# Performance work log

Hardware: AMD Instinct MI355X
Metric: run time of the kernel (lower is better)

Reference implementation:

```python
import jax, jax.numpy as jnp
import numpy as np

NEG = -1e30  # log-space 'zero' (avoid actual -inf for stable grads)
BLANK = 1


def _ctc_single(logp, target, il, tl):
    # logp: [T, V] log-probabilities; target: [S] int; il, tl: scalar lengths
    T, V = logp.shape
    S = target.shape[0]
    L = 2 * S + 1
    # extended label sequence: blank, t0, blank, t1, ..., blank
    ext = jnp.full((L,), BLANK, dtype=target.dtype).at[1::2].set(target)
    prev2 = jnp.concatenate([jnp.full((2,), -1, dtype=ext.dtype), ext[:-2]])
    can_skip = (ext != BLANK) & (ext != prev2)  # allowed s-2 transition
    valid = jnp.arange(L) < (2 * tl + 1)  # mask lattice positions beyond target length
    lp_ext = logp[:, ext]  # [T, L] gather of emission log-probs along the lattice

    alpha0 = jnp.full((L,), NEG, dtype=logp.dtype)
    alpha0 = alpha0.at[0].set(lp_ext[0, 0]).at[1].set(lp_ext[0, 1])
    alpha0 = jnp.where(valid, alpha0, NEG)

    def step(alpha, inp):
        t, lp = inp  # lp: [L]
        a1 = jnp.concatenate([jnp.full((1,), NEG, alpha.dtype), alpha[:-1]])
        a2 = jnp.concatenate([jnp.full((2,), NEG, alpha.dtype), alpha[:-2]])
        a2 = jnp.where(can_skip, a2, NEG)
        new = jnp.logaddexp(jnp.logaddexp(alpha, a1), a2) + lp
        new = jnp.where(valid, new, NEG)
        new = jnp.where(t < il, new, alpha)  # freeze alpha past input length
        return new, None

    alpha, _ = jax.lax.scan(step, alpha0, (jnp.arange(1, T), lp_ext[1:]))
    end = 2 * tl
    ll = jnp.logaddexp(alpha[end], alpha[end - 1])
    loss = -ll
    # zero_infinity=True: clamp non-finite / degenerate losses to 0
    loss = jnp.where(loss < 1e29, loss, 0.0)
    return loss


def setup_inputs() -> dict:
    key = jax.random.key(0)
    k1, k2, k3, k4 = jax.random.split(key, 4)
    B, T, V, S = 64, 2000, 256, 400
    # module expects log-probabilities over phonemes
    log_probs = jax.nn.log_softmax(
        jax.random.normal(k1, (B, T, V), dtype=jnp.float32), axis=-1)
    # targets avoid blank_id=1 (labels in [2, V))
    targets = jax.random.randint(k2, (B, S), 2, V, dtype=jnp.int32)
    input_lengths = jax.random.randint(k3, (B,), T // 2, T + 1, dtype=jnp.int32)
    target_lengths = jax.random.randint(k4, (B,), S // 2, S + 1, dtype=jnp.int32)
    return {"log_probs": log_probs, "targets": targets,
            "input_lengths": input_lengths, "target_lengths": target_lengths}


def reference(log_probs, targets, input_lengths, target_lengths):
    losses = jax.vmap(_ctc_single)(log_probs, targets, input_lengths, target_lengths)
    # nn.CTCLoss reduction='mean': per-sample loss divided by target length, then batch mean
    return jnp.mean(losses / target_lengths.astype(losses.dtype))
```

## Files before the change

kernel.cpp:

```cpp
#include <hip/hip_runtime.h>

#define LOG2E 1.4426950408889634f
#define LN2   0.6931471805599453f

namespace {
constexpr int B    = 64;
constexpr int T    = 2000;
constexpr int V    = 256;
constexpr int S    = 400;
constexpr int CHK  = 8;
constexpr int NCTP = 250;
constexpr int KP   = 408;
constexpr size_t GELEM  = (size_t)B * NCTP * KP * 8;
constexpr size_t GBYTES = GELEM * 2;
constexpr size_t LAOFF  = GBYTES / 4;
constexpr size_t LGOFF  = LAOFF + 64 * 1024;
constexpr size_t REQBYTES = GBYTES + 2 * 64 * 1024 * 4;
constexpr int LSTR = 260;
constexpr int NW7  = 7;
constexpr int NCT7 = 250;
constexpr int BST7 = 12;
}

using h8 = __attribute__((ext_vector_type(8))) _Float16;

__device__ __forceinline__ float fexp2(float x){ return __builtin_amdgcn_exp2f(x); }
__device__ __forceinline__ float flog2(float x){ return __builtin_amdgcn_logf(x); }

__device__ __forceinline__ float wave_shr1(float x) {
  int v = __builtin_amdgcn_update_dpp(0, __builtin_bit_cast(int, x),
                                      0x138, 0xf, 0xf, true);
  return __builtin_bit_cast(float, v);
}
__device__ __forceinline__ int wave_shr1_i(int x) {
  return __builtin_amdgcn_update_dpp(0, x, 0x138, 0xf, 0xf, true);
}
__device__ __forceinline__ float wave_shl1(float x) {
  int v = __builtin_amdgcn_update_dpp(0, __builtin_bit_cast(int, x),
                                      0x130, 0xf, 0xf, true);
  return __builtin_bit_cast(float, v);
}
__device__ __forceinline__ int wave_shl1_i(int x) {
  return __builtin_amdgcn_update_dpp(0, x, 0x130, 0xf, 0xf, true);
}

__global__ __launch_bounds__(512)
void ctc_gather_kernel(const float* __restrict__ logp,
                       const int* __restrict__ targets,
                       _Float16* __restrict__ G)
{
  const int tile = blockIdx.x;
  const int b    = blockIdx.y;
  const int tid  = threadIdx.x;
  const int i0   = tile * 64;
  const float* lp = logp + (size_t)b * T * V;
  const int*   tg = targets + (size_t)b * S;

  __shared__ float ls[64 * LSTR];
  __shared__ int   tgs[S];

  for (int f = tid; f < 64 * 64; f += 512) {
    const int row = f >> 6, c4 = f & 63;
    int t = i0 + 1 + row; if (t > T - 1) t = T - 1;
    float4 v = ((const float4*)(lp + (size_t)t * V))[c4];
    *(float4*)&ls[row * LSTR + c4 * 4] = v;
  }
  for (int k = tid; k < S; k += 512) tgs[k] = tg[k];
  __syncthreads();

  const int w    = tid >> 6;
  const int lane = tid & 63;
  _Float16* gb = G + (size_t)b * NCTP * KP * 8;

  for (int it = w; it < 64; it += 8) {
    const int cc = it >> 3;
    const int j  = it & 7;
    const int c  = tile * 8 + cc;
    if (c >= NCTP) continue;
    if (lane > 50) continue;
    const int k = 8 * lane + j;
    const int e = (k < S) ? tgs[k] : 1;
    h8 hv;
    #pragma unroll
    for (int jj = 0; jj < 8; ++jj)
      hv[jj] = (_Float16)fexp2(ls[(cc * 8 + jj) * LSTR + e] * LOG2E);
    *(h8*)(gb + ((size_t)c * KP + j * 51 + lane) * 8) = hv;
  }
}

__global__ __launch_bounds__(64)
void ctc_fb_kernel(const float* __restrict__ logp,
                   const int* __restrict__ targets,
                   const int* __restrict__ input_len,
                   const int* __restrict__ target_len,
                   const _Float16* __restrict__ G,
                   float* __restrict__ la,
                   float* __restrict__ lg)
{
  const int b    = blockIdx.x;
  const int dir  = blockIdx.y;
  const int lane = threadIdx.x & 63;
  const float* __restrict__ lp = logp + (size_t)b * T * V;
  const int il = input_len[b];
  const int tl = target_len[b];
  const int m  = il >> 1;
  const int* tg = targets + (size_t)b * S;

  const _Float16* Gb = G + (size_t)b * NCTP * KP * 8;
  const int lclamp = (lane < 50) ? lane : 50;

  float skF[8], skB[8];
  #pragma unroll
  for (int j = 0; j < 8; ++j) {
    const int k   = 8 * lane + j;
    const int kc  = k < S ? k : S - 1;
    const int km  = (k - 1) < 0 ? 0 : ((k - 1) < S ? (k - 1) : S - 1);
    skF[j] = (k > 0 && tg[kc] != tg[km]) ? 1.0f : 0.0f;
    const int k2  = k + 1;
    const int k2c = k2 < S ? k2 : S - 1;
    const int k2m = (k2 - 1) < S ? (k2 - 1) : S - 1;
    skB[j] = (tg[k2c] != tg[k2m]) ? 1.0f : 0.0f;
  }

  h8 bufA[9], bufB[9];

  auto loadch = [&](h8 (&buf)[9], int c2) {
    if (c2 < 0) c2 = 0;
    if (c2 > NCTP - 1) c2 = NCTP - 1;
    const _Float16* src = Gb + (size_t)c2 * (KP * 8);
    #pragma unroll
    for (int j = 0; j < 8; ++j)
      buf[j] = *(const h8*)(src + (size_t)(j * 51 + lclamp) * 8);
    buf[8] = *(const h8*)(src + (size_t)50 * 8);
  };

  if (dir == 0) {
    float a[16];
    #pragma unroll
    for (int i = 0; i < 16; ++i) a[i] = 0.0f;
    int  E = 0;
    bool alive = (lane == 0);
    if (lane == 0) {
      a[0] = fexp2(lp[1] * LOG2E);
      a[1] = fexp2(lp[tg[0]] * LOG2E);
    }

    auto fwd_sub = [&](h8 (&buf)[9], const int c_) {
      h8 cur[9];
      #pragma unroll
      for (int r = 0; r < 9; ++r) cur[r] = buf[r];
      loadch(buf, c_ + 2);

      const int E1 = wave_shr1_i(E);
      if (!alive) E = E1;
      int d = E1 - E; d = d > 126 ? 126 : (d < -126 ? -126 : d);
      const float f = ldexpf(1.0f, d);

      #pragma unroll
      for (int i = 0; i < 8; ++i) {
        const int t = 1 + c_ * CHK + i;
        if (t <= m) {
          const float pbi = (float)cur[8][i];
          const float h = wave_shr1(a[15]) * f;
          #pragma unroll
          for (int j = 7; j >= 0; --j) {
            const float psj = (float)cur[j][i];
            const float lo = j ? a[2 * j - 1] : h;
            a[2 * j + 1] = __builtin_fmaf(lo, skF[j],
                                          a[2 * j + 1] + a[2 * j]) * psj;
            a[2 * j]     = (a[2 * j] + lo) * pbi;
          }
        }
      }
      {
        float mx[8];
        #pragma unroll
        for (int q = 0; q < 8; ++q) mx[q] = fmaxf(a[2 * q], a[2 * q + 1]);
        #pragma unroll
        for (int q = 0; q < 4; ++q) mx[q] = fmaxf(mx[q], mx[q + 4]);
        const float m2 = fmaxf(fmaxf(mx[0], mx[1]), fmaxf(mx[2], mx[3]));
        int k = 0; (void)frexpf(m2, &k);
        #pragma unroll
        for (int i = 0; i < 16; ++i) a[i] = ldexpf(a[i], -k);
        E += k;
        alive = (m2 != 0.0f);
      }
    };

    loadch(bufA, 0); loadch(bufB, 1);
    const int NCH = (m + 7) >> 3;
    for (int c = 0; c < NCH; c += 2) {
      fwd_sub(bufA, c);
      fwd_sub(bufB, c + 1);
    }

    float* dst = la + (size_t)b * 1024 + 16 * lane;
    #pragma unroll
    for (int i = 0; i < 16; ++i) dst[i] = flog2(a[i]) + (float)E;
  } else {
    float g[16];
    const int s0 = 16 * lane;
    bool alive = false;
    #pragma unroll
    for (int i = 0; i < 16; ++i) {
      const int s = s0 + i;
      g[i] = (s == 2 * tl || s == 2 * tl - 1) ? 1.0f : 0.0f;
      alive = alive || (g[i] != 0.0f);
    }
    int E = 0;

    const int c_hi = (il - 2) >> 3;
    const int c_lo = m >> 3;

    auto bwd_sub = [&](h8 (&buf)[9], const int c_) {
      h8 cur[9];
      #pragma unroll
      for (int r = 0; r < 9; ++r) cur[r] = buf[r];
      loadch(buf, c_ - 2);

      const int E1 = wave_shl1_i(E);
      if (!alive) E = E1;
      int d = E1 - E; d = d > 126 ? 126 : (d < -126 ? -126 : d);
      const float f = ldexpf(1.0f, d);

      #pragma unroll
      for (int ii = 0; ii < 8; ++ii) {
        const int i = 7 - ii;
        const int row = 1 + c_ * CHK + i;
        if (row > m && row < il) {
          const float pbi = (float)cur[8][i];
          float pg[16];
          #pragma unroll
          for (int q = 0; q < 8; ++q) {
            pg[2 * q]     = g[2 * q]     * pbi;
            pg[2 * q + 1] = g[2 * q + 1] * (float)cur[q][i];
          }
          const float h0 = wave_shl1(pg[0]) * f;
          const float h1 = wave_shl1(pg[1]) * f;
          #pragma unroll
          for (int q = 0; q < 8; ++q) {
            const float u1 = (q < 7) ? pg[2 * q + 2] : h0;
            const float u2 = (q < 7) ? pg[2 * q + 3] : h1;
            g[2 * q + 1] = __builtin_fmaf(u2, skB[q], pg[2 * q + 1] + u1);
            g[2 * q]     = pg[2 * q] + pg[2 * q + 1];
          }
        }
      }
      {
        float mx[8];
        #pragma unroll
        for (int q = 0; q < 8; ++q) mx[q] = fmaxf(g[2 * q], g[2 * q + 1]);
        #pragma unroll
        for (int q = 0; q < 4; ++q) mx[q] = fmaxf(mx[q], mx[q + 4]);
        const float m2 = fmaxf(fmaxf(mx[0], mx[1]), fmaxf(mx[2], mx[3]));
        int k = 0; (void)frexpf(m2, &k);
        #pragma unroll
        for (int i = 0; i < 16; ++i) g[i] = ldexpf(g[i], -k);
        E += k;
        alive = (m2 != 0.0f);
      }
    };

    loadch(bufA, c_hi); loadch(bufB, c_hi - 1);
    for (int c = c_hi; c >= c_lo; c -= 2) {
      bwd_sub(bufA, c);
      bwd_sub(bufB, c - 1);
    }

    float* dst = lg + (size_t)b * 1024 + 16 * lane;
    #pragma unroll
    for (int i = 0; i < 16; ++i) dst[i] = flog2(g[i]) + (float)E;
  }
}

__global__ __launch_bounds__(64)
void ctc_merge_kernel(const float* __restrict__ la,
                      const float* __restrict__ lg,
                      const int* __restrict__ target_len,
                      float* __restrict__ out)
{
  const int b    = blockIdx.x;
  const int lane = threadIdx.x;
  const int tl = target_len[b];
  const int Lb = 2 * tl + 1;
  const float* A  = la + (size_t)b * 1024;
  const float* Gm = lg + (size_t)b * 1024;

  float vs[16];
  float vmax = -1e30f;
  #pragma unroll
  for (int r = 0; r < 16; ++r) {
    const int s = lane + 64 * r;
    float x = A[s] + Gm[s];
    x = (s < Lb) ? x : -1e30f;
    vs[r] = x;
    vmax = fmaxf(vmax, x);
  }
  #pragma unroll
  for (int o = 32; o > 0; o >>= 1) vmax = fmaxf(vmax, __shfl_xor(vmax, o, 64));
  float sum = 0.0f;
  #pragma unroll
  for (int r = 0; r < 16; ++r) sum += fexp2(vs[r] - vmax);
  #pragma unroll
  for (int o = 32; o > 0; o >>= 1) sum += __shfl_xor(sum, o, 64);
  if (lane == 0) {
    const float ll = (vmax + flog2(sum)) * LN2;
    float loss = -ll;
    if (!(loss < 1e29f)) loss = 0.0f;
    atomicAdd(out, loss / ((float)tl * (float)B));
  }
}

__global__ __launch_bounds__(NW7 * 64)
void ctc_alpha7_kernel(const float* __restrict__ logp,
                       const int* __restrict__ targets,
                       const int* __restrict__ input_len,
                       const int* __restrict__ target_len,
                       float* __restrict__ out)
{
  const int b    = blockIdx.x;
  const int tid  = threadIdx.x;
  const int w    = tid >> 6;
  const int lane = tid & 63;
  const bool lane0 = (lane == 0);
  const float* __restrict__ lp = logp + (size_t)b * T * V;
  const int il = input_len[b];
  const int tl = target_len[b];
  const int Lb = 2 * tl + 1;

  __shared__ float bnd[NW7 - 1][NCT7 * BST7];
  __shared__ int   cnt[NW7 - 1];
  __shared__ float pblk[T];
  __shared__ float afin[NW7 * 64 * 2];

  if (tid < NW7 - 1) cnt[tid] = 0;

  const int* tg = targets + (size_t)b * S;
  const int k1 = (tid < S) ? tid : (S - 1);
  const int e1 = tg[k1];
  const float sk1 = (k1 == 0 || e1 != tg[k1 - 1]) ? 1.0f : 0.0f;

  for (int i = tid; i < T; i += NW7 * 64) {
    int t = (i + 1 < T) ? (i + 1) : (T - 1);
    pblk[i] = fexp2(lp[(size_t)t * V + 1] * LOG2E);
  }
  __syncthreads();

  const bool active = (w * 128) < Lb;
  if (active) {
    float a0 = 0.0f, a1 = 0.0f;
    int   E  = 0;
    if (tid == 0) { a0 = fexp2(lp[1] * LOG2E); a1 = fexp2(lp[e1] * LOG2E); }

    float tokL[CHK];
    #pragma unroll
    for (int i = 0; i < CHK; ++i) tokL[i] = lp[(size_t)(1 + i) * V + e1];

    const int NCH = (il - 1 + CHK - 1) / CHK;
    for (int c = 0; c < NCH; ++c) {
      const int t0 = 1 + c * CHK;
      float tokP[CHK];
      #pragma unroll
      for (int i = 0; i < CHK; ++i) tokP[i] = fexp2(tokL[i] * LOG2E);
      float nl[CHK];
      if (c + 1 < NCT7) {
        #pragma unroll
        for (int i = 0; i < CHK; ++i) {
          int tt = t0 + CHK + i; if (tt > T - 1) tt = T - 1;
          nl[i] = lp[(size_t)tt * V + e1];
        }
      }
      float pbk[CHK];
      {
        float4 q0 = *(const float4*)&pblk[c * CHK];
        float4 q1 = *(const float4*)&pblk[c * CHK + 4];
        pbk[0]=q0.x; pbk[1]=q0.y; pbk[2]=q0.z; pbk[3]=q0.w;
        pbk[4]=q1.x; pbk[5]=q1.y; pbk[6]=q1.z; pbk[7]=q1.w;
      }
      float bq[CHK];
      int Ep = 0;
      if (w > 0) {
        while (__hip_atomic_load(&cnt[w - 1], __ATOMIC_ACQUIRE,
                                 __HIP_MEMORY_SCOPE_WORKGROUP) < c + 1)
          __builtin_amdgcn_s_sleep(1);
        const float* src = &bnd[w - 1][c * BST7];
        float4 q0 = *(const float4*)(src);
        float4 q1 = *(const float4*)(src + 4);
        bq[0]=q0.x; bq[1]=q0.y; bq[2]=q0.z; bq[3]=q0.w;
        bq[4]=q1.x; bq[5]=q1.y; bq[6]=q1.z; bq[7]=q1.w;
        Ep = __float_as_int(src[8]);
      } else {
        #pragma unroll
        for (int i = 0; i < CHK; ++i) bq[i] = 0.0f;
      }
      const float mz  = fmaxf(a0, a1);
      const int   E1o = __shfl_up(E, 1);
      const int   E8  = __shfl_up(E, 8);
      const int   E9  = __shfl_up(E, 9);
      const float mz1 = __shfl_up(mz, 1);
      if (mz == 0.0f) E = (lane < 8) ? Ep : E8;
      int E1 = (mz1 == 0.0f) ? ((lane <= 8) ? Ep : E9) : E1o;
      if (lane0) E1 = (w == 0) ? E : Ep;
      int d = E1 - E; d = d > 126 ? 126 : (d < -126 ? -126 : d);
      const float f = ldexpf(1.0f, d);
      const float a1s = a1;
      float pub[CHK];
      #pragma unroll
      for (int i = 0; i < CHK; ++i) {
        const int t = t0 + i;
        if (t < il) {
          float hl = wave_shr1(a1);
          hl = lane0 ? bq[i] : hl;
          hl *= f;
          float s01 = a1 + a0;
          a1 = __builtin_fmaf(hl, sk1, s01) * tokP[i];
          a0 = (a0 + hl) * pbk[i];
        }
        pub[i] = a1;
      }
      if (w < NW7 - 1 && lane == 63) {
        float* dst = &bnd[w][c * BST7];
        dst[0] = a1s;
        #pragma unroll
        for (int i = 0; i < CHK - 1; ++i) dst[1 + i] = pub[i];
        dst[8] = __int_as_float(E);
        __hip_atomic_store(&cnt[w], c + 1, __ATOMIC_RELEASE,
                           __HIP_MEMORY_SCOPE_WORKGROUP);
      }
      {
        float m2 = fmaxf(a0, a1);
        int k = 0;
        (void)frexpf(m2, &k);
        a0 = ldexpf(a0, -k);
        a1 = ldexpf(a1, -k);
        E += k;
      }
      #pragma unroll
      for (int i = 0; i < CHK; ++i) tokL[i] = nl[i];
    }
    afin[2 * tid]     = flog2(a0) + (float)E;
    afin[2 * tid + 1] = flog2(a1) + (float)E;
  }
  __syncthreads();

  if (tid == 0) {
    const float x = afin[2 * tl];
    const float y = afin[2 * tl - 1];
    const float mm = fmaxf(x, y);
    const float ll = (mm + flog2(fexp2(x - mm) + fexp2(y - mm))) * LN2;
    float loss = -ll;
    if (!(loss < 1e29f)) loss = 0.0f;
    atomicAdd(out, loss / ((float)tl * (float)B));
  }
}

__global__ void ctc_zero_kernel(float* __restrict__ out) { out[0] = 0.0f; }

extern "C" void kernel_launch(void* const* d_in, const int* in_sizes, int n_in,
                              void* d_out, int out_size, void* d_ws, size_t ws_size,
                              hipStream_t stream) {
  const float* logp    = (const float*)d_in[0];
  const int*   targets = (const int*)d_in[1];
  const int*   il      = (const int*)d_in[2];
  const int*   tl      = (const int*)d_in[3];
  float* out = (float*)d_out;

  ctc_zero_kernel<<<1, 1, 0, stream>>>(out);
  if (ws_size >= REQBYTES) {
    _Float16* G  = (_Float16*)d_ws;
    float*    la = (float*)d_ws + LAOFF;
    float*    lg = (float*)d_ws + LGOFF;
    ctc_gather_kernel<<<dim3(32, B), 512, 0, stream>>>(logp, targets, G);
    ctc_fb_kernel<<<dim3(B, 2), 64, 0, stream>>>(logp, targets, il, tl, G, la, lg);
    ctc_merge_kernel<<<B, 64, 0, stream>>>(la, lg, tl, out);
  } else {
    ctc_alpha7_kernel<<<B, NW7 * 64, 0, stream>>>(logp, targets, il, tl, out);
  }
}
```

Baseline: 341.4 us.

## Fuse emission gather into forward-backward kernel via LDS double-buffered rows

Removes the separate gather kernel that precomputed fp16 exp-emissions into a large workspace. Instead, each forward/backward wave streams raw log-prob rows for its 8-step chunk, exponentiates them and writes them into a double-buffered LDS table. The recurrence then indexes that table by target label. This drops one kernel launch and the global round trip of the gathered table, and keeps emissions in fp32. In exchange, every wave now runs exp on all 256 vocab entries per step, LDS gathers may bank-conflict, and only 128 single-wave blocks run, so the streaming load latency sits on the serial critical path.

```diff
diff --git a/kernel.cpp b/kernel.cpp
--- a/kernel.cpp
+++ b/kernel.cpp
@@ -10,19 +10,12 @@
 constexpr int S    = 400;
 constexpr int CHK  = 8;
 constexpr int NCTP = 250;
-constexpr int KP   = 408;
-constexpr size_t GELEM  = (size_t)B * NCTP * KP * 8;
-constexpr size_t GBYTES = GELEM * 2;
-constexpr size_t LAOFF  = GBYTES / 4;
-constexpr size_t LGOFF  = LAOFF + 64 * 1024;
-constexpr size_t REQBYTES = GBYTES + 2 * 64 * 1024 * 4;
-constexpr int LSTR = 260;
+constexpr size_t LGOFF    = 64 * 1024;
+constexpr size_t REQBYTES = 2 * 64 * 1024 * 4;
 constexpr int NW7  = 7;
 constexpr int NCT7 = 250;
 constexpr int BST7 = 12;
 }
-
-using h8 = __attribute__((ext_vector_type(8))) _Float16;
 
 __device__ __forceinline__ float fexp2(float x){ return __builtin_amdgcn_exp2f(x); }
 __device__ __forceinline__ float flog2(float x){ return __builtin_amdgcn_logf(x); }
@@ -42,50 +35,6 @@
 }
 __device__ __forceinline__ int wave_shl1_i(int x) {
   return __builtin_amdgcn_update_dpp(0, x, 0x130, 0xf, 0xf, true);
-}
-
-__global__ __launch_bounds__(512)
-void ctc_gather_kernel(const float* __restrict__ logp,
-                       const int* __restrict__ targets,
-                       _Float16* __restrict__ G)
-{
-  const int tile = blockIdx.x;
-  const int b    = blockIdx.y;
-  const int tid  = threadIdx.x;
-  const int i0   = tile * 64;
-  const float* lp = logp + (size_t)b * T * V;
-  const int*   tg = targets + (size_t)b * S;
-
-  __shared__ float ls[64 * LSTR];
-  __shared__ int   tgs[S];
-
-  for (int f = tid; f < 64 * 64; f += 512) {
-    const int row = f >> 6, c4 = f & 63;
-    int t = i0 + 1 + row; if (t > T - 1) t = T - 1;
-    float4 v = ((const float4*)(lp + (size_t)t * V))[c4];
-    *(float4*)&ls[row * LSTR + c4 * 4] = v;
-  }
-  for (int k = tid; k < S; k += 512) tgs[k] = tg[k];
-  __syncthreads();
-
-  const int w    = tid >> 6;
-  const int lane = tid & 63;
-  _Float16* gb = G + (size_t)b * NCTP * KP * 8;
-
-  for (int it = w; it < 64; it += 8) {
-    const int cc = it >> 3;
-    const int j  = it & 7;
-    const int c  = tile * 8 + cc;
-    if (c >= NCTP) continue;
-    if (lane > 50) continue;
-    const int k = 8 * lane + j;
-    const int e = (k < S) ? tgs[k] : 1;
-    h8 hv;
-    #pragma unroll
-    for (int jj = 0; jj < 8; ++jj)
-      hv[jj] = (_Float16)fexp2(ls[(cc * 8 + jj) * LSTR + e] * LOG2E);
-    *(h8*)(gb + ((size_t)c * KP + j * 51 + lane) * 8) = hv;
-  }
 }
 
 __global__ __launch_bounds__(64)
@@ -93,7 +42,6 @@
                    const int* __restrict__ targets,
                    const int* __restrict__ input_len,
                    const int* __restrict__ target_len,
-                   const _Float16* __restrict__ G,
                    float* __restrict__ la,
                    float* __restrict__ lg)
 {
@@ -106,15 +54,16 @@
   const int m  = il >> 1;
   const int* tg = targets + (size_t)b * S;
 
-  const _Float16* Gb = G + (size_t)b * NCTP * KP * 8;
-  const int lclamp = (lane < 50) ? lane : 50;
-
+  __shared__ float tbl[2][CHK * V];
+
+  int   ecol[8];
   float skF[8], skB[8];
   #pragma unroll
   for (int j = 0; j < 8; ++j) {
     const int k   = 8 * lane + j;
     const int kc  = k < S ? k : S - 1;
     const int km  = (k - 1) < 0 ? 0 : ((k - 1) < S ? (k - 1) : S - 1);
+    ecol[j] = tg[kc];
     skF[j] = (k > 0 && tg[kc] != tg[km]) ? 1.0f : 0.0f;
     const int k2  = k + 1;
     const int k2c = k2 < S ? k2 : S - 1;
@@ -122,16 +71,29 @@
     skB[j] = (tg[k2c] != tg[k2m]) ? 1.0f : 0.0f;
   }
 
-  h8 bufA[9], bufB[9];
-
-  auto loadch = [&](h8 (&buf)[9], int c2) {
+  float4 st[8];
+  auto issue = [&](int c2) {
     if (c2 < 0) c2 = 0;
     if (c2 > NCTP - 1) c2 = NCTP - 1;
-    const _Float16* src = Gb + (size_t)c2 * (KP * 8);
-    #pragma unroll
-    for (int j = 0; j < 8; ++j)
-      buf[j] = *(const h8*)(src + (size_t)(j * 51 + lclamp) * 8);
-    buf[8] = *(const h8*)(src + (size_t)50 * 8);
+    #pragma unroll
+    for (int q = 0; q < 8; ++q) {
+      int r = 1 + 8 * c2 + q; if (r > T - 1) r = T - 1;
+      st[q] = *(const float4*)(lp + (size_t)r * V + 4 * lane);
+    }
+    __builtin_amdgcn_sched_barrier(0);
+  };
+  auto commit = [&](int slot) {
+    #pragma unroll
+    for (int q = 0; q < 8; ++q) {
+      float4 v;
+      v.x = fexp2(st[q].x * LOG2E);
+      v.y = fexp2(st[q].y * LOG2E);
+      v.z = fexp2(st[q].z * LOG2E);
+      v.w = fexp2(st[q].w * LOG2E);
+      *(float4*)&tbl[slot][q * V + 4 * lane] = v;
+    }
+    asm volatile("s_waitcnt lgkmcnt(0)" ::: "memory");
+    __builtin_amdgcn_sched_barrier(0);
   };
 
   if (dir == 0) {
@@ -145,11 +107,11 @@
       a[1] = fexp2(lp[tg[0]] * LOG2E);
     }
 
-    auto fwd_sub = [&](h8 (&buf)[9], const int c_) {
-      h8 cur[9];
-      #pragma unroll
-      for (int r = 0; r < 9; ++r) cur[r] = buf[r];
-      loadch(buf, c_ + 2);
+    issue(0); commit(0);
+    const int NCH = (m + 7) >> 3;
+    for (int n = 0; n < NCH; ++n) {
+      issue(n + 1);
+      const float* __restrict__ rowb = &tbl[n & 1][0];
 
       const int E1 = wave_shr1_i(E);
       if (!alive) E = E1;
@@ -158,13 +120,14 @@
 
       #pragma unroll
       for (int i = 0; i < 8; ++i) {
-        const int t = 1 + c_ * CHK + i;
+        const int t = 1 + n * CHK + i;
         if (t <= m) {
-          const float pbi = (float)cur[8][i];
+          const float* __restrict__ row = rowb + i * V;
+          const float pbi = row[1];
           const float h = wave_shr1(a[15]) * f;
           #pragma unroll
           for (int j = 7; j >= 0; --j) {
-            const float psj = (float)cur[j][i];
+            const float psj = row[ecol[j]];
             const float lo = j ? a[2 * j - 1] : h;
             a[2 * j + 1] = __builtin_fmaf(lo, skF[j],
                                           a[2 * j + 1] + a[2 * j]) * psj;
@@ -185,13 +148,7 @@
         E += k;
         alive = (m2 != 0.0f);
       }
-    };
-
-    loadch(bufA, 0); loadch(bufB, 1);
-    const int NCH = (m + 7) >> 3;
-    for (int c = 0; c < NCH; c += 2) {
-      fwd_sub(bufA, c);
-      fwd_sub(bufB, c + 1);
+      commit((n + 1) & 1);
     }
 
     float* dst = la + (size_t)b * 1024 + 16 * lane;
@@ -212,11 +169,10 @@
     const int c_hi = (il - 2) >> 3;
     const int c_lo = m >> 3;
 
-    auto bwd_sub = [&](h8 (&buf)[9], const int c_) {
-      h8 cur[9];
-      #pragma unroll
-      for (int r = 0; r < 9; ++r) cur[r] = buf[r];
-      loadch(buf, c_ - 2);
+    issue(c_hi); commit(c_hi & 1);
+    for (int n = c_hi; n >= c_lo; --n) {
+      issue(n - 1);
+      const float* __restrict__ rowb = &tbl[n & 1][0];
 
       const int E1 = wave_shl1_i(E);
       if (!alive) E = E1;
@@ -226,14 +182,15 @@
       #pragma unroll
       for (int ii = 0; ii < 8; ++ii) {
         const int i = 7 - ii;
-        const int row = 1 + c_ * CHK + i;
-        if (row > m && row < il) {
-          const float pbi = (float)cur[8][i];
+        const int row_t = 1 + n * CHK + i;
+        if (row_t > m && row_t < il) {
+          const float* __restrict__ row = rowb + i * V;
+          const float pbi = row[1];
           float pg[16];
           #pragma unroll
           for (int q = 0; q < 8; ++q) {
             pg[2 * q]     = g[2 * q]     * pbi;
-            pg[2 * q + 1] = g[2 * q + 1] * (float)cur[q][i];
+            pg[2 * q + 1] = g[2 * q + 1] * row[ecol[q]];
           }
           const float h0 = wave_shl1(pg[0]) * f;
           const float h1 = wave_shl1(pg[1]) * f;
@@ -259,12 +216,7 @@
         E += k;
         alive = (m2 != 0.0f);
       }
-    };
-
-    loadch(bufA, c_hi); loadch(bufB, c_hi - 1);
-    for (int c = c_hi; c >= c_lo; c -= 2) {
-      bwd_sub(bufA, c);
-      bwd_sub(bufB, c - 1);
+      commit((n - 1) & 1);
     }
 
     float* dst = lg + (size_t)b * 1024 + 16 * lane;
@@ -467,11 +419,9 @@
 
   ctc_zero_kernel<<<1, 1, 0, stream>>>(out);
   if (ws_size >= REQBYTES) {
-    _Float16* G  = (_Float16*)d_ws;
-    float*    la = (float*)d_ws + LAOFF;
-    float*    lg = (float*)d_ws + LGOFF;
-    ctc_gather_kernel<<<dim3(32, B), 512, 0, stream>>>(logp, targets, G);
-    ctc_fb_kernel<<<dim3(B, 2), 64, 0, stream>>>(logp, targets, il, tl, G, la, lg);
+    float* la = (float*)d_ws;
+    float* lg = (float*)d_ws + LGOFF;
+    ctc_fb_kernel<<<dim3(B, 2), 64, 0, stream>>>(logp, targets, il, tl, la, lg);
     ctc_merge_kernel<<<B, 64, 0, stream>>>(la, lg, tl, out);
   } else {
     ctc_alpha7_kernel<<<B, NW7 * 64, 0, stream>>>(logp, targets, il, tl, out);
```

Result: slower. 441.4 us (+29.3%).

## Stream emission chunks through a 4-deep LDS ring via async global_load_lds

Applied to the files above, without the earlier changes.

The register double-buffer of per-chunk emission data is replaced by a four-slot shared-memory ring filled with global_load_lds, with hand-placed vmcnt and lgkmcnt waits. Chunks are now prefetched four ahead, which hides more global-load latency on the serial recurrence. The ring also frees the VGPRs the second register buffer used. In exchange each chunk costs extra LDS reads, and correctness depends on the manual waitcnt counts (vmcnt 21 assumes exactly 7 loads per chunk).

```diff
diff --git a/kernel.cpp b/kernel.cpp
--- a/kernel.cpp
+++ b/kernel.cpp
@@ -44,6 +44,13 @@
   return __builtin_amdgcn_update_dpp(0, x, 0x130, 0xf, 0xf, true);
 }
 
+#define WAITVM21() do { asm volatile("s_waitcnt vmcnt(21)" ::: "memory"); \
+                        __builtin_amdgcn_sched_barrier(0); } while (0)
+#define WAITVM0()  do { asm volatile("s_waitcnt vmcnt(0)"  ::: "memory"); \
+                        __builtin_amdgcn_sched_barrier(0); } while (0)
+#define WARGUARD() do { asm volatile("s_waitcnt lgkmcnt(0)" ::: "memory"); \
+                        __builtin_amdgcn_sched_barrier(0); } while (0)
+
 __global__ __launch_bounds__(512)
 void ctc_gather_kernel(const float* __restrict__ logp,
                        const int* __restrict__ targets,
@@ -122,16 +129,27 @@
     skB[j] = (tg[k2c] != tg[k2m]) ? 1.0f : 0.0f;
   }
 
-  h8 bufA[9], bufB[9];
-
-  auto loadch = [&](h8 (&buf)[9], int c2) {
+  __shared__ alignas(16) _Float16 ring[4][448 * 8];
+
+  auto stage = [&](int c2, int slot) {
     if (c2 < 0) c2 = 0;
     if (c2 > NCTP - 1) c2 = NCTP - 1;
     const _Float16* src = Gb + (size_t)c2 * (KP * 8);
     #pragma unroll
+    for (int i = 0; i < 7; ++i) {
+      int p = i * 64 + lane; if (p > KP - 1) p = KP - 1;
+      __builtin_amdgcn_global_load_lds(src + (size_t)p * 8,
+                                       &ring[slot][(size_t)i * 64 * 8],
+                                       16, 0, 0);
+    }
+  };
+
+  auto rdchunk = [&](int slot, h8 (&cur)[9]) {
+    const _Float16* sl = &ring[slot][0];
+    #pragma unroll
     for (int j = 0; j < 8; ++j)
-      buf[j] = *(const h8*)(src + (size_t)(j * 51 + lclamp) * 8);
-    buf[8] = *(const h8*)(src + (size_t)50 * 8);
+      cur[j] = *(const h8*)(sl + (size_t)(j * 51 + lclamp) * 8);
+    cur[8] = *(const h8*)(sl + (size_t)50 * 8);
   };
 
   if (dir == 0) {
@@ -145,11 +163,14 @@
       a[1] = fexp2(lp[tg[0]] * LOG2E);
     }
 
-    auto fwd_sub = [&](h8 (&buf)[9], const int c_) {
-      h8 cur[9];
-      #pragma unroll
-      for (int r = 0; r < 9; ++r) cur[r] = buf[r];
-      loadch(buf, c_ + 2);
+    WAITVM0();
+    stage(0, 0); stage(1, 1); stage(2, 2); stage(3, 3);
+
+    h8 cur[9];
+    const int NCH = (m + 7) >> 3;
+    for (int n = 0; n < NCH; ++n) {
+      WAITVM21();
+      rdchunk(n & 3, cur);
 
       const int E1 = wave_shr1_i(E);
       if (!alive) E = E1;
@@ -158,7 +179,7 @@
 
       #pragma unroll
       for (int i = 0; i < 8; ++i) {
-        const int t = 1 + c_ * CHK + i;
+        const int t = 1 + n * CHK + i;
         if (t <= m) {
           const float pbi = (float)cur[8][i];
           const float h = wave_shr1(a[15]) * f;
@@ -185,13 +206,9 @@
         E += k;
         alive = (m2 != 0.0f);
       }
-    };
-
-    loadch(bufA, 0); loadch(bufB, 1);
-    const int NCH = (m + 7) >> 3;
-    for (int c = 0; c < NCH; c += 2) {
-      fwd_sub(bufA, c);
-      fwd_sub(bufB, c + 1);
+
+      WARGUARD();
+      stage(n + 4, n & 3);
     }
 
     float* dst = la + (size_t)b * 1024 + 16 * lane;
@@ -212,11 +229,14 @@
     const int c_hi = (il - 2) >> 3;
     const int c_lo = m >> 3;
 
-    auto bwd_sub = [&](h8 (&buf)[9], const int c_) {
-      h8 cur[9];
-      #pragma unroll
-      for (int r = 0; r < 9; ++r) cur[r] = buf[r];
-      loadch(buf, c_ - 2);
+    WAITVM0();
+    stage(c_hi, c_hi & 3);         stage(c_hi - 1, (c_hi - 1) & 3);
+    stage(c_hi - 2, (c_hi - 2) & 3); stage(c_hi - 3, (c_hi - 3) & 3);
+
+    h8 cur[9];
+    for (int n = c_hi; n >= c_lo; --n) {
+      WAITVM21();
+      rdchunk(n & 3, cur);
 
       const int E1 = wave_shl1_i(E);
       if (!alive) E = E1;
@@ -226,8 +246,8 @@
       #pragma unroll
       for (int ii = 0; ii < 8; ++ii) {
         const int i = 7 - ii;
-        const int row = 1 + c_ * CHK + i;
-        if (row > m && row < il) {
+        const int row_t = 1 + n * CHK + i;
+        if (row_t > m && row_t < il) {
           const float pbi = (float)cur[8][i];
           float pg[16];
           #pragma unroll
@@ -259,12 +279,9 @@
         E += k;
         alive = (m2 != 0.0f);
       }
-    };
-
-    loadch(bufA, c_hi); loadch(bufB, c_hi - 1);
-    for (int c = c_hi; c >= c_lo; c -= 2) {
-      bwd_sub(bufA, c);
-      bwd_sub(bufB, c - 1);
+
+      WARGUARD();
+      stage(n - 4, n & 3);
     }
 
     float* dst = lg + (size_t)b * 1024 + 16 * lane;
```

Result: slower. 366.6 us (+7.4%).

## Interleave two batch samples per wave in forward-backward CTC kernel

Applied to the files above, without the earlier changes.

Each wave now runs the alpha (or beta) recurrence for two batch elements together, interleaving their steps so the two independent dependency chains can hide each other's latency (cross-lane shifts, FMA chains). The grid is halved to 64 waves total, and the double-buffered chunk prefetch is replaced by a single buffer per sample that is reloaded after each chunk. This raises ILP but halves wave-level parallelism, adds register pressure, and makes each pair run as long as its longer sample.

```diff
diff --git a/kernel.cpp b/kernel.cpp
--- a/kernel.cpp
+++ b/kernel.cpp
@@ -97,179 +97,195 @@
                    float* __restrict__ la,
                    float* __restrict__ lg)
 {
-  const int b    = blockIdx.x;
+  const int b0   = 2 * blockIdx.x;
+  const int b1   = b0 + 1;
   const int dir  = blockIdx.y;
   const int lane = threadIdx.x & 63;
-  const float* __restrict__ lp = logp + (size_t)b * T * V;
-  const int il = input_len[b];
-  const int tl = target_len[b];
-  const int m  = il >> 1;
-  const int* tg = targets + (size_t)b * S;
-
-  const _Float16* Gb = G + (size_t)b * NCTP * KP * 8;
+  const float* __restrict__ lp0 = logp + (size_t)b0 * T * V;
+  const float* __restrict__ lp1 = logp + (size_t)b1 * T * V;
+  const int il0 = input_len[b0],  il1 = input_len[b1];
+  const int tl0 = target_len[b0], tl1 = target_len[b1];
+  const int m0  = il0 >> 1,       m1  = il1 >> 1;
+  const int* tg0 = targets + (size_t)b0 * S;
+  const int* tg1 = targets + (size_t)b1 * S;
+
+  const _Float16* Gb0 = G + (size_t)b0 * NCTP * KP * 8;
+  const _Float16* Gb1 = G + (size_t)b1 * NCTP * KP * 8;
   const int lclamp = (lane < 50) ? lane : 50;
 
-  float skF[8], skB[8];
-  #pragma unroll
-  for (int j = 0; j < 8; ++j) {
-    const int k   = 8 * lane + j;
-    const int kc  = k < S ? k : S - 1;
-    const int km  = (k - 1) < 0 ? 0 : ((k - 1) < S ? (k - 1) : S - 1);
-    skF[j] = (k > 0 && tg[kc] != tg[km]) ? 1.0f : 0.0f;
-    const int k2  = k + 1;
-    const int k2c = k2 < S ? k2 : S - 1;
-    const int k2m = (k2 - 1) < S ? (k2 - 1) : S - 1;
-    skB[j] = (tg[k2c] != tg[k2m]) ? 1.0f : 0.0f;
-  }
-
-  h8 bufA[9], bufB[9];
-
-  auto loadch = [&](h8 (&buf)[9], int c2) {
+  auto loadch = [&](h8 (&buf)[9], const _Float16* Gbase, int c2) {
     if (c2 < 0) c2 = 0;
     if (c2 > NCTP - 1) c2 = NCTP - 1;
-    const _Float16* src = Gb + (size_t)c2 * (KP * 8);
+    const _Float16* src = Gbase + (size_t)c2 * (KP * 8);
     #pragma unroll
     for (int j = 0; j < 8; ++j)
       buf[j] = *(const h8*)(src + (size_t)(j * 51 + lclamp) * 8);
     buf[8] = *(const h8*)(src + (size_t)50 * 8);
   };
 
+  auto renorm = [&](float (&a)[16], int &E, bool &alive) {
+    float mx[8];
+    #pragma unroll
+    for (int q = 0; q < 8; ++q) mx[q] = fmaxf(a[2 * q], a[2 * q + 1]);
+    #pragma unroll
+    for (int q = 0; q < 4; ++q) mx[q] = fmaxf(mx[q], mx[q + 4]);
+    const float m2 = fmaxf(fmaxf(mx[0], mx[1]), fmaxf(mx[2], mx[3]));
+    int k = 0; (void)frexpf(m2, &k);
+    #pragma unroll
+    for (int i = 0; i < 16; ++i) a[i] = ldexpf(a[i], -k);
+    E += k;
+    alive = (m2 != 0.0f);
+  };
+
   if (dir == 0) {
-    float a[16];
-    #pragma unroll
-    for (int i = 0; i < 16; ++i) a[i] = 0.0f;
-    int  E = 0;
-    bool alive = (lane == 0);
+    float skF0[8], skF1[8];
+    #pragma unroll
+    for (int j = 0; j < 8; ++j) {
+      const int k  = 8 * lane + j;
+      const int kc = k < S ? k : S - 1;
+      const int km = (k - 1) < 0 ? 0 : ((k - 1) < S ? (k - 1) : S - 1);
+      skF0[j] = (k > 0 && tg0[kc] != tg0[km]) ? 1.0f : 0.0f;
+      skF1[j] = (k > 0 && tg1[kc] != tg1[km]) ? 1.0f : 0.0f;
+    }
+
+    float a0[16], a1[16];
+    #pragma unroll
+    for (int i = 0; i < 16; ++i) { a0[i] = 0.0f; a1[i] = 0.0f; }
+    int  E0 = 0, E1 = 0;
+    bool alive0 = (lane == 0), alive1 = (lane == 0);
     if (lane == 0) {
-      a[0] = fexp2(lp[1] * LOG2E);
-      a[1] = fexp2(lp[tg[0]] * LOG2E);
-    }
-
-    auto fwd_sub = [&](h8 (&buf)[9], const int c_) {
-      h8 cur[9];
-      #pragma unroll
-      for (int r = 0; r < 9; ++r) cur[r] = buf[r];
-      loadch(buf, c_ + 2);
-
-      const int E1 = wave_shr1_i(E);
-      if (!alive) E = E1;
-      int d = E1 - E; d = d > 126 ? 126 : (d < -126 ? -126 : d);
-      const float f = ldexpf(1.0f, d);
-
+      a0[0] = fexp2(lp0[1] * LOG2E);  a0[1] = fexp2(lp0[tg0[0]] * LOG2E);
+      a1[0] = fexp2(lp1[1] * LOG2E);  a1[1] = fexp2(lp1[tg1[0]] * LOG2E);
+    }
+
+    auto eexF = [&](int &E, bool alive) -> float {
+      const int En = wave_shr1_i(E);
+      if (!alive) E = En;
+      int d = En - E; d = d > 126 ? 126 : (d < -126 ? -126 : d);
+      return ldexpf(1.0f, d);
+    };
+    auto fstep = [&](float (&a)[16], const float (&sk)[8], h8 (&cur)[9],
+                     float f, int i) {
+      const float pbi = (float)cur[8][i];
+      const float h = wave_shr1(a[15]) * f;
+      #pragma unroll
+      for (int j = 7; j >= 0; --j) {
+        const float psj = (float)cur[j][i];
+        const float lo = j ? a[2 * j - 1] : h;
+        a[2 * j + 1] = __builtin_fmaf(lo, sk[j],
+                                      a[2 * j + 1] + a[2 * j]) * psj;
+        a[2 * j]     = (a[2 * j] + lo) * pbi;
+      }
+    };
+
+    h8 buf0[9], buf1[9];
+    loadch(buf0, Gb0, 0); loadch(buf1, Gb1, 0);
+    const int NCH0 = (m0 + 7) >> 3, NCH1 = (m1 + 7) >> 3;
+    const int NCH = NCH0 > NCH1 ? NCH0 : NCH1;
+    for (int n = 0; n < NCH; ++n) {
+      const float f0 = eexF(E0, alive0);
+      const float f1 = eexF(E1, alive1);
       #pragma unroll
       for (int i = 0; i < 8; ++i) {
-        const int t = 1 + c_ * CHK + i;
-        if (t <= m) {
-          const float pbi = (float)cur[8][i];
-          const float h = wave_shr1(a[15]) * f;
-          #pragma unroll
-          for (int j = 7; j >= 0; --j) {
-            const float psj = (float)cur[j][i];
-            const float lo = j ? a[2 * j - 1] : h;
-            a[2 * j + 1] = __builtin_fmaf(lo, skF[j],
-                                          a[2 * j + 1] + a[2 * j]) * psj;
-            a[2 * j]     = (a[2 * j] + lo) * pbi;
-          }
-        }
-      }
-      {
-        float mx[8];
-        #pragma unroll
-        for (int q = 0; q < 8; ++q) mx[q] = fmaxf(a[2 * q], a[2 * q + 1]);
-        #pragma unroll
-        for (int q = 0; q < 4; ++q) mx[q] = fmaxf(mx[q], mx[q + 4]);
-        const float m2 = fmaxf(fmaxf(mx[0], mx[1]), fmaxf(mx[2], mx[3]));
-        int k = 0; (void)frexpf(m2, &k);
-        #pragma unroll
-        for (int i = 0; i < 16; ++i) a[i] = ldexpf(a[i], -k);
-        E += k;
-        alive = (m2 != 0.0f);
-      }
-    };
-
-    loadch(bufA, 0); loadch(bufB, 1);
-    const int NCH = (m + 7) >> 3;
-    for (int c = 0; c < NCH; c += 2) {
-      fwd_sub(bufA, c);
-      fwd_sub(bufB, c + 1);
-    }
-
-    float* dst = la + (size_t)b * 1024 + 16 * lane;
-    #pragma unroll
-    for (int i = 0; i < 16; ++i) dst[i] = flog2(a[i]) + (float)E;
+        const int t = 1 + n * CHK + i;
+        if (t <= m0) fstep(a0, skF0, buf0, f0, i);
+        if (t <= m1) fstep(a1, skF1, buf1, f1, i);
+      }
+      loadch(buf0, Gb0, n + 1);
+      loadch(buf1, Gb1, n + 1);
+      renorm(a0, E0, alive0);
+      renorm(a1, E1, alive1);
+    }
+
+    float* d0 = la + (size_t)b0 * 1024 + 16 * lane;
+    float* d1 = la + (size_t)b1 * 1024 + 16 * lane;
+    #pragma unroll
+    for (int i = 0; i < 16; ++i) {
+      d0[i] = flog2(a0[i]) + (float)E0;
+      d1[i] = flog2(a1[i]) + (float)E1;
+    }
   } else {
-    float g[16];
+    float skB0[8], skB1[8];
+    #pragma unroll
+    for (int j = 0; j < 8; ++j) {
+      const int k2  = 8 * lane + j + 1;
+      const int k2c = k2 < S ? k2 : S - 1;
+      const int k2m = (k2 - 1) < S ? (k2 - 1) : S - 1;
+      skB0[j] = (tg0[k2c] != tg0[k2m]) ? 1.0f : 0.0f;
+      skB1[j] = (tg1[k2c] != tg1[k2m]) ? 1.0f : 0.0f;
+    }
+
+    float g0[16], g1[16];
     const int s0 = 16 * lane;
-    bool alive = false;
+    bool alive0 = false, alive1 = false;
     #pragma unroll
     for (int i = 0; i < 16; ++i) {
       const int s = s0 + i;
-      g[i] = (s == 2 * tl || s == 2 * tl - 1) ? 1.0f : 0.0f;
-      alive = alive || (g[i] != 0.0f);
-    }
-    int E = 0;
-
-    const int c_hi = (il - 2) >> 3;
-    const int c_lo = m >> 3;
-
-    auto bwd_sub = [&](h8 (&buf)[9], const int c_) {
-      h8 cur[9];
-      #pragma unroll
-      for (int r = 0; r < 9; ++r) cur[r] = buf[r];
-      loadch(buf, c_ - 2);
-
-      const int E1 = wave_shl1_i(E);
-      if (!alive) E = E1;
-      int d = E1 - E; d = d > 126 ? 126 : (d < -126 ? -126 : d);
-      const float f = ldexpf(1.0f, d);
-
+      g0[i] = (s == 2 * tl0 || s == 2 * tl0 - 1) ? 1.0f : 0.0f;
+      g1[i] = (s == 2 * tl1 || s == 2 * tl1 - 1) ? 1.0f : 0.0f;
+      alive0 = alive0 || (g0[i] != 0.0f);
+      alive1 = alive1 || (g1[i] != 0.0f);
+    }
+    int E0 = 0, E1 = 0;
+
+    auto eexB = [&](int &E, bool alive) -> float {
+      const int En = wave_shl1_i(E);
+      if (!alive) E = En;
+      int d = En - E; d = d > 126 ? 126 : (d < -126 ? -126 : d);
+      return ldexpf(1.0f, d);
+    };
+    auto bstep = [&](float (&g)[16], const float (&sk)[8], h8 (&cur)[9],
+                     float f, int i) {
+      const float pbi = (float)cur[8][i];
+      float pg[16];
+      #pragma unroll
+      for (int q = 0; q < 8; ++q) {
+        pg[2 * q]     = g[2 * q]     * pbi;
+        pg[2 * q + 1] = g[2 * q + 1] * (float)cur[q][i];
+      }
+      const float h0 = wave_shl1(pg[0]) * f;
+      const float h1 = wave_shl1(pg[1]) * f;
+      #pragma unroll
+      for (int q = 0; q < 8; ++q) {
+        const float u1 = (q < 7) ? pg[2 * q + 2] : h0;
+        const float u2 = (q < 7) ? pg[2 * q + 3] : h1;
+        g[2 * q + 1] = __builtin_fmaf(u2, sk[q], pg[2 * q + 1] + u1);
+        g[2 * q]     = pg[2 * q] + pg[2 * q + 1];
+      }
+    };
+
+    const int c_hi0 = (il0 - 2) >> 3, c_lo0 = m0 >> 3;
+    const int c_hi1 = (il1 - 2) >> 3, c_lo1 = m1 >> 3;
+    const int span0 = c_hi0 - c_lo0, span1 = c_hi1 - c_lo1;
+    const int SPAN = span0 > span1 ? span0 : span1;
+
+    h8 buf0[9], buf1[9];
+    loadch(buf0, Gb0, c_hi0); loadch(buf1, Gb1, c_hi1);
+    for (int it = 0; it <= SPAN; ++it) {
+      const int n0 = c_hi0 - it, n1 = c_hi1 - it;
+      const float f0 = eexB(E0, alive0);
+      const float f1 = eexB(E1, alive1);
       #pragma unroll
       for (int ii = 0; ii < 8; ++ii) {
         const int i = 7 - ii;
-        const int row = 1 + c_ * CHK + i;
-        if (row > m && row < il) {
-          const float pbi = (float)cur[8][i];
-          float pg[16];
-          #pragma unroll
-          for (int q = 0; q < 8; ++q) {
-            pg[2 * q]     = g[2 * q]     * pbi;
-            pg[2 * q + 1] = g[2 * q + 1] * (float)cur[q][i];
-          }
-          const float h0 = wave_shl1(pg[0]) * f;
-          const float h1 = wave_shl1(pg[1]) * f;
-          #pragma unroll
-          for (int q = 0; q < 8; ++q) {
-            const float u1 = (q < 7) ? pg[2 * q + 2] : h0;
-            const float u2 = (q < 7) ? pg[2 * q + 3] : h1;
-            g[2 * q + 1] = __builtin_fmaf(u2, skB[q], pg[2 * q + 1] + u1);
-            g[2 * q]     = pg[2 * q] + pg[2 * q + 1];
-          }
-        }
-      }
-      {
-        float mx[8];
-        #pragma unroll
-        for (int q = 0; q < 8; ++q) mx[q] = fmaxf(g[2 * q], g[2 * q + 1]);
-        #pragma unroll
-        for (int q = 0; q < 4; ++q) mx[q] = fmaxf(mx[q], mx[q + 4]);
-        const float m2 = fmaxf(fmaxf(mx[0], mx[1]), fmaxf(mx[2], mx[3]));
-        int k = 0; (void)frexpf(m2, &k);
-        #pragma unroll
-        for (int i = 0; i < 16; ++i) g[i] = ldexpf(g[i], -k);
-        E += k;
-        alive = (m2 != 0.0f);
-      }
-    };
-
-    loadch(bufA, c_hi); loadch(bufB, c_hi - 1);
-    for (int c = c_hi; c >= c_lo; c -= 2) {
-      bwd_sub(bufA, c);
-      bwd_sub(bufB, c - 1);
-    }
-
-    float* dst = lg + (size_t)b * 1024 + 16 * lane;
-    #pragma unroll
-    for (int i = 0; i < 16; ++i) dst[i] = flog2(g[i]) + (float)E;
+        const int r0 = 1 + n0 * CHK + i;
+        const int r1 = 1 + n1 * CHK + i;
+        if (r0 > m0 && r0 < il0) bstep(g0, skB0, buf0, f0, i);
+        if (r1 > m1 && r1 < il1) bstep(g1, skB1, buf1, f1, i);
+      }
+      loadch(buf0, Gb0, n0 - 1);
+      loadch(buf1, Gb1, n1 - 1);
+      renorm(g0, E0, alive0);
+      renorm(g1, E1, alive1);
+    }
+
+    float* d0 = lg + (size_t)b0 * 1024 + 16 * lane;
+    float* d1 = lg + (size_t)b1 * 1024 + 16 * lane;
+    #pragma unroll
+    for (int i = 0; i < 16; ++i) {
+      d0[i] = flog2(g0[i]) + (float)E0;
+      d1[i] = flog2(g1[i]) + (float)E1;
+    }
   }
 }
 
@@ -471,7 +487,7 @@
     float*    la = (float*)d_ws + LAOFF;
     float*    lg = (float*)d_ws + LGOFF;
     ctc_gather_kernel<<<dim3(32, B), 512, 0, stream>>>(logp, targets, G);
-    ctc_fb_kernel<<<dim3(B, 2), 64, 0, stream>>>(logp, targets, il, tl, G, la, lg);
+    ctc_fb_kernel<<<dim3(B / 2, 2), 64, 0, stream>>>(logp, targets, il, tl, G, la, lg);
     ctc_merge_kernel<<<B, 64, 0, stream>>>(la, lg, tl, out);
   } else {
     ctc_alpha7_kernel<<<B, NW7 * 64, 0, stream>>>(logp, targets, il, tl, out);
```

New measurement: 578.2 us. +69.4%, slower.
